# Kernel optimization log

Measured on AMD Instinct MI355X. Metric: run time of the kernel, lower is better.

## Reference

```python
import jax, jax.numpy as jnp
import numpy as np

B, S, D, H = 2, 2048, 1024, 16
DH = D // H
LEVELS, FACTOR = 3, 2


def setup_inputs() -> dict:
    key = jax.random.key(0)
    ks = jax.random.split(key, 12)
    s = 1.0 / np.sqrt(D)
    n = lambda k, shape, sc: (jax.random.normal(k, shape, jnp.float32) * sc)
    return {
        "query": n(ks[0], (B, S, D), 1.0),
        "key": n(ks[1], (B, S, D), 1.0),
        "value": n(ks[2], (B, S, D), 1.0),
        "Wq": n(ks[3], (D, D), s), "bq": jnp.zeros((D,), jnp.float32),
        "Wk": n(ks[4], (D, D), s), "bk": jnp.zeros((D,), jnp.float32),
        "Wv": n(ks[5], (D, D), s), "bv": jnp.zeros((D,), jnp.float32),
        "Wo": n(ks[6], (D, D), s), "bo": jnp.zeros((D,), jnp.float32),
        "w_levels": jnp.ones((LEVELS,), jnp.float32),
    }


def _downsample(m):
    # mean-pool pairs along sequence: [B, S, D] -> [B, S//FACTOR, D]
    b, s, d = m.shape
    sn = s // FACTOR
    return m[:, : sn * FACTOR, :].reshape(b, sn, FACTOR, d).mean(axis=2)


def _mha(q, k, v, Wq, bq, Wk, bk, Wv, bv, Wo, bo):
    b, sq, d = q.shape
    sk = k.shape[1]
    qh = (q @ Wq + bq).reshape(b, sq, H, DH)
    kh = (k @ Wk + bk).reshape(b, sk, H, DH)
    vh = (v @ Wv + bv).reshape(b, sk, H, DH)
    scores = jnp.einsum("bqhd,bkhd->bhqk", qh, kh) / np.sqrt(DH)
    attn = jax.nn.softmax(scores, axis=-1)
    out = jnp.einsum("bhqk,bkhd->bqhd", attn, vh).reshape(b, sq, d)
    return out @ Wo + bo


def reference(query, key, value, Wq, bq, Wk, bk, Wv, bv, Wo, bo, w_levels):
    keys, vals = [key], [value]
    k_, v_ = key, value
    for _ in range(LEVELS - 1):
        k_ = _downsample(k_)
        v_ = _downsample(v_)
        keys.append(k_)
        vals.append(v_)
    acc = None
    for lvl in range(LEVELS):
        o = _mha(query, keys[lvl], vals[lvl], Wq, bq, Wk, bk, Wv, bv, Wo, bo)
        o = o * w_levels[lvl]
        acc = o if acc is None else acc + o
    return acc / w_levels.sum()
```

## Files before the change

kernel.cpp:

```cpp
#include <hip/hip_runtime.h>


#define B_  2
#define S_  2048
#define D_  1024
#define H_  16
#define DH_ 64
#define THR2 10.0f

typedef short s8v __attribute__((ext_vector_type(8)));
typedef float f4v __attribute__((ext_vector_type(4)));
typedef float f16v __attribute__((ext_vector_type(16)));
typedef unsigned int u32x2 __attribute__((ext_vector_type(2)));
typedef unsigned int u32x4 __attribute__((ext_vector_type(4)));

__device__ __forceinline__ unsigned cvtpk(float lo, float hi){
    unsigned r;
    asm volatile("v_cvt_pk_bf16_f32 %0, %1, %2" : "=v"(r) : "v"(lo), "v"(hi));
    return r;
}
__device__ __forceinline__ unsigned short f2bf1(float v){
    unsigned r;
    asm volatile("v_cvt_pk_bf16_f32 %0, %1, %2" : "=v"(r) : "v"(v), "v"(v));
    return (unsigned short)r;
}
__device__ __forceinline__ float bf2f(unsigned short h){
    union { unsigned u; float f; } v; v.u = ((unsigned)h) << 16;
    return v.f;
}
__device__ __forceinline__ float exp2_(float x){
    float r; asm("v_exp_f32 %0, %1" : "=v"(r) : "v"(x)); return r;
}
__device__ __forceinline__ void pswap(unsigned &dst, unsigned &src){
    asm volatile("v_permlane32_swap_b32 %0, %1" : "+v"(dst), "+v"(src));
}
__device__ __forceinline__ unsigned addpk(unsigned x, unsigned y){
    union { unsigned u; float f; } a, b, c, d;
    a.u = x << 16;          b.u = y << 16;
    c.u = x & 0xFFFF0000u;  d.u = y & 0xFFFF0000u;
    return cvtpk(a.f + b.f, c.f + d.f);
}
__device__ __forceinline__ int swz(int row, int kb){
    return row*128 + (((kb) ^ (row & 7) ^ ((row >> 3) & 7)) << 4);
}

__global__ __launch_bounds__(256) void wtrans(
    const float* __restrict__ W0, const float* __restrict__ W1,
    const float* __restrict__ W2, const float* __restrict__ W3,
    unsigned short* __restrict__ T0, unsigned short* __restrict__ T1,
    unsigned short* __restrict__ T2, unsigned short* __restrict__ T3)
{
    __shared__ float tl[32][33];
    const float* W = blockIdx.z==0?W0: blockIdx.z==1?W1: blockIdx.z==2?W2:W3;
    unsigned short* T = blockIdx.z==0?T0: blockIdx.z==1?T1: blockIdx.z==2?T2:T3;
    const int t = threadIdx.x;
    const int bk = blockIdx.x*32, bn = blockIdx.y*32;
    {
        int row = t>>3, c4 = (t&7)*4;
        float4 v = *(const float4*)&W[(size_t)(bk+row)*D_ + bn + c4];
        tl[row][c4+0]=v.x; tl[row][c4+1]=v.y; tl[row][c4+2]=v.z; tl[row][c4+3]=v.w;
    }
    __syncthreads();
    {
        int n = t>>3, k4 = (t&7)*4;
        unsigned a = cvtpk(tl[k4+0][n], tl[k4+1][n]);
        unsigned b = cvtpk(tl[k4+2][n], tl[k4+3][n]);
        u32x2 pk = {a, b};
        *(u32x2*)&T[(size_t)(bn+n)*D_ + bk + k4] = pk;
    }
}

template<int MODE>
__global__ __launch_bounds__(256) void gemm_proj(
    const float* __restrict__ Af, const unsigned short* __restrict__ Btw,
    const float* __restrict__ bias, unsigned short* __restrict__ C, float scale)
{
    const int N_ = D_, K_ = D_;
    __shared__ __align__(16) char lds[65536];
    const int t = threadIdx.x;
    const int l = t & 63, wv = t>>6, g = l>>4, x = l&15;
    const int wr = wv>>1, wc = wv&1;
    const int br = blockIdx.y*128, bc = blockIdx.x*128;

    int rw[4], bl[4];
    #pragma unroll
    for (int p=0;p<4;++p){ int u = t + 256*p; rw[p] = u>>3; bl[p] = u&7; }

    f4v acc[4][4];
    #pragma unroll
    for (int i=0;i<4;++i)
        #pragma unroll
        for (int j=0;j<4;++j) acc[i][j] = (f4v){0.f,0.f,0.f,0.f};

    float4 alo[4], ahi[4]; s8v brg[4];
    #pragma unroll
    for (int p=0;p<4;++p){
        const float* ap = Af + (size_t)(br+rw[p])*K_ + bl[p]*8;
        alo[p] = *(const float4*)ap; ahi[p] = *(const float4*)(ap+4);
        brg[p] = *(const s8v*)(Btw + (size_t)(bc+rw[p])*K_ + bl[p]*8);
    }

    int cur = 0;
    for (int kt=0; kt<K_; kt+=64){
        char* AsB = lds + cur*32768;
        char* BsB = AsB + 16384;
        #pragma unroll
        for (int p=0;p<4;++p){
            uint4 pk;
            pk.x = cvtpk(alo[p].x, alo[p].y); pk.y = cvtpk(alo[p].z, alo[p].w);
            pk.z = cvtpk(ahi[p].x, ahi[p].y); pk.w = cvtpk(ahi[p].z, ahi[p].w);
            *(uint4*)(AsB + swz(rw[p], bl[p])) = pk;
            *(s8v*)(BsB + swz(rw[p], bl[p])) = brg[p];
        }
        if (kt + 64 < K_){
            #pragma unroll
            for (int p=0;p<4;++p){
                const float* ap = Af + (size_t)(br+rw[p])*K_ + (kt+64) + bl[p]*8;
                alo[p] = *(const float4*)ap; ahi[p] = *(const float4*)(ap+4);
                brg[p] = *(const s8v*)(Btw + (size_t)(bc+rw[p])*K_ + (kt+64) + bl[p]*8);
            }
        }
        __syncthreads();
        #pragma unroll
        for (int c=0;c<2;++c){
            s8v af[4], bf[4];
            #pragma unroll
            for (int fm=0; fm<4; ++fm)
                af[fm] = *(const s8v*)(AsB + swz(wr*64+fm*16+x, c*4+g));
            #pragma unroll
            for (int fn=0; fn<4; ++fn)
                bf[fn] = *(const s8v*)(BsB + swz(wc*64+fn*16+x, c*4+g));
            __builtin_amdgcn_s_setprio(1);
            #pragma unroll
            for (int fm=0; fm<4; ++fm)
                #pragma unroll
                for (int fn=0; fn<4; ++fn)
                    acc[fm][fn] = __builtin_amdgcn_mfma_f32_16x16x32_bf16(
                        af[fm], bf[fn], acc[fm][fn], 0,0,0);
            __builtin_amdgcn_s_setprio(0);
        }
        cur ^= 1;
    }

    #pragma unroll
    for (int fn=0; fn<4; ++fn){
        int col = bc + wc*64 + fn*16 + x;
        float bv = bias[col];
        #pragma unroll
        for (int fm=0; fm<4; ++fm){
            int row0 = br + wr*64 + fm*16 + g*4;
            float v0 = acc[fm][fn][0] + bv;
            float v1 = acc[fm][fn][1] + bv;
            float v2 = acc[fm][fn][2] + bv;
            float v3 = acc[fm][fn][3] + bv;
            if (MODE == 1){
                int hI = col>>6, dhI = col & (DH_-1);
                #pragma unroll
                for (int r=0;r<4;++r){
                    int row = row0 + r;
                    int bI = row>>11, sI = row & (S_-1);
                    float vv = (r==0?v0: r==1?v1: r==2?v2: v3) * scale;
                    C[(((size_t)(bI*H_+hI))*S_+sI)*DH_+dhI] = f2bf1(vv);
                }
            } else {
                int bI = row0>>11, sI = row0 & (S_-1);
                int hI = col>>6, dhI = col & (DH_-1);
                u32x2 pk;
                pk.x = cvtpk(v0*scale, v1*scale);
                pk.y = cvtpk(v2*scale, v3*scale);
                *(u32x2*)&C[(((size_t)(bI*H_+hI))*DH_+dhI)*S_ + sI] = pk;
            }
        }
    }
}

__global__ __launch_bounds__(256) void gemm_sum(
    const unsigned short* __restrict__ A0, const unsigned short* __restrict__ A1,
    const unsigned short* __restrict__ Btw, const float* __restrict__ bias,
    float* __restrict__ C)
{
    const int N_ = D_, K_ = D_;
    __shared__ __align__(16) char lds[65536];
    const int t = threadIdx.x;
    const int l = t & 63, wv = t>>6, g = l>>4, x = l&15;
    const int wr = wv>>1, wc = wv&1;
    const int br = blockIdx.y*128, bc = blockIdx.x*128;

    int rw[4], bl[4];
    #pragma unroll
    for (int p=0;p<4;++p){ int u = t + 256*p; rw[p] = u>>3; bl[p] = u&7; }

    f4v acc[4][4];
    #pragma unroll
    for (int i=0;i<4;++i)
        #pragma unroll
        for (int j=0;j<4;++j) acc[i][j] = (f4v){0.f,0.f,0.f,0.f};

    u32x4 a0r[4], a1r[4]; s8v brg[4];
    #pragma unroll
    for (int p=0;p<4;++p){
        a0r[p] = *(const u32x4*)(A0 + (size_t)(br+rw[p])*K_ + bl[p]*8);
        a1r[p] = *(const u32x4*)(A1 + (size_t)(br+rw[p])*K_ + bl[p]*8);
        brg[p] = *(const s8v*)(Btw + (size_t)(bc+rw[p])*K_ + bl[p]*8);
    }

    int cur = 0;
    for (int kt=0; kt<K_; kt+=64){
        char* AsB = lds + cur*32768;
        char* BsB = AsB + 16384;
        #pragma unroll
        for (int p=0;p<4;++p){
            uint4 pk;
            pk.x = addpk(a0r[p].x, a1r[p].x);
            pk.y = addpk(a0r[p].y, a1r[p].y);
            pk.z = addpk(a0r[p].z, a1r[p].z);
            pk.w = addpk(a0r[p].w, a1r[p].w);
            *(uint4*)(AsB + swz(rw[p], bl[p])) = pk;
            *(s8v*)(BsB + swz(rw[p], bl[p])) = brg[p];
        }
        if (kt + 64 < K_){
            #pragma unroll
            for (int p=0;p<4;++p){
                a0r[p] = *(const u32x4*)(A0 + (size_t)(br+rw[p])*K_ + (kt+64) + bl[p]*8);
                a1r[p] = *(const u32x4*)(A1 + (size_t)(br+rw[p])*K_ + (kt+64) + bl[p]*8);
                brg[p] = *(const s8v*)(Btw + (size_t)(bc+rw[p])*K_ + (kt+64) + bl[p]*8);
            }
        }
        __syncthreads();
        #pragma unroll
        for (int c=0;c<2;++c){
            s8v af[4], bf[4];
            #pragma unroll
            for (int fm=0; fm<4; ++fm)
                af[fm] = *(const s8v*)(AsB + swz(wr*64+fm*16+x, c*4+g));
            #pragma unroll
            for (int fn=0; fn<4; ++fn)
                bf[fn] = *(const s8v*)(BsB + swz(wc*64+fn*16+x, c*4+g));
            __builtin_amdgcn_s_setprio(1);
            #pragma unroll
            for (int fm=0; fm<4; ++fm)
                #pragma unroll
                for (int fn=0; fn<4; ++fn)
                    acc[fm][fn] = __builtin_amdgcn_mfma_f32_16x16x32_bf16(
                        af[fm], bf[fn], acc[fm][fn], 0,0,0);
            __builtin_amdgcn_s_setprio(0);
        }
        cur ^= 1;
    }

    #pragma unroll
    for (int fn=0; fn<4; ++fn){
        int col = bc + wc*64 + fn*16 + x;
        float bv = bias[col];
        #pragma unroll
        for (int fm=0; fm<4; ++fm){
            int row0 = br + wr*64 + fm*16 + g*4;
            #pragma unroll
            for (int r=0;r<4;++r)
                C[(size_t)(row0+r)*N_ + col] = acc[fm][fn][r] + bv;
        }
    }
}

__global__ __launch_bounds__(256) void pool_pair(
    const unsigned short* __restrict__ kin, unsigned short* __restrict__ kout,
    const unsigned short* __restrict__ vin, unsigned short* __restrict__ vout,
    int nOut4, int Sin, int shift)
{
    int idx = blockIdx.x * 256 + threadIdx.x;
    if (idx >= nOut4) return;
    if (blockIdx.z == 0){
        int d0 = (idx & 15) * 4;
        int rest = idx >> 4;
        int Sout = Sin >> 1;
        int so = rest % Sout, bh = rest / Sout;
        size_t base = ((size_t)bh * Sin + 2*so) * DH_ + d0;
        ushort4 a = *(const ushort4*)&kin[base];
        ushort4 c = *(const ushort4*)&kin[base + DH_];
        ushort4 o;
        o.x = f2bf1(0.5f*(bf2f(a.x)+bf2f(c.x)));
        o.y = f2bf1(0.5f*(bf2f(a.y)+bf2f(c.y)));
        o.z = f2bf1(0.5f*(bf2f(a.z)+bf2f(c.z)));
        o.w = f2bf1(0.5f*(bf2f(a.w)+bf2f(c.w)));
        *(ushort4*)&kout[(size_t)idx*4] = o;
    } else {
        int row = idx >> shift;
        int so4 = (idx & ((1<<shift)-1)) << 2;
        union { u32x4 u; unsigned short hh[8]; } a;
        a.u = *(const u32x4*)&vin[(size_t)row*Sin + so4*2];
        float m0 = 0.5f*(bf2f(a.hh[0])+bf2f(a.hh[1]));
        float m1 = 0.5f*(bf2f(a.hh[2])+bf2f(a.hh[3]));
        float m2 = 0.5f*(bf2f(a.hh[4])+bf2f(a.hh[5]));
        float m3 = 0.5f*(bf2f(a.hh[6])+bf2f(a.hh[7]));
        u32x2 pk; pk.x = cvtpk(m0,m1); pk.y = cvtpk(m2,m3);
        *(u32x2*)&vout[(size_t)row*(Sin>>1) + so4] = pk;
    }
}

__global__ __launch_bounds__(256, 2) void attn_mfma7(
    const unsigned short* __restrict__ qh,
    const unsigned short* __restrict__ kh0, const unsigned short* __restrict__ kh1,
    const unsigned short* __restrict__ kh2,
    const unsigned short* __restrict__ vt0, const unsigned short* __restrict__ vt1,
    const unsigned short* __restrict__ vt2,
    const float* __restrict__ wlv,
    unsigned short* __restrict__ acc0, unsigned short* __restrict__ acc1)
{
    __shared__ __align__(16) char ksm[2][8192];
    __shared__ __align__(16) char vsm[2][8192];
    const int t = threadIdx.x, l = t&63, wv = t>>6, q = l&31, hi = l>>5;
    const int bid = blockIdx.x;
    const int qt = bid & 15, h = (bid>>4) & (H_-1), b = bid >> 8;
    const int grp = blockIdx.y;
    const int lvB = grp ? 1 : 0, lvE = grp ? 3 : 1;
    unsigned short* accOut = grp ? acc1 : acc0;

    const float w0 = wlv[0], w1 = wlv[1], w2 = wlv[2];
    const float winv = 1.f/(w0+w1+w2);

    const unsigned short* qp =
        qh + (((size_t)(b*H_+h))*S_ + (size_t)qt*128 + wv*32 + q)*DH_ + hi*8;
    s8v qf0 = *(const s8v*)(qp);
    s8v qf1 = *(const s8v*)(qp + 16);
    s8v qf2 = *(const s8v*)(qp + 32);
    s8v qf3 = *(const s8v*)(qp + 48);

    const int r0 = t>>3, kb = t&7;
    const int off0 = swz(r0, kb), off1 = swz(r0+32, kb);

    f16v aO0, aO1;
    #pragma unroll
    for (int r=0;r<16;++r){ aO0[r]=0.f; aO1[r]=0.f; }

    int cur = 0;
    #pragma unroll 1
    for (int lvl = lvB; lvl < lvE; ++lvl) {
        const unsigned short *kp, *vpt; int nt; float wc;
        if (lvl == 0)      { kp = kh0; vpt = vt0; nt = 32; wc = w0; }
        else if (lvl == 1) { kp = kh1; vpt = vt1; nt = 16; wc = w1; }
        else               { kp = kh2; vpt = vt2; nt = 8;  wc = w2; }
        const int Sl = nt*64;
        const unsigned short* kbase = kp + (size_t)(b*H_+h)*Sl*DH_;
        const unsigned short* v0r = vpt + ((size_t)(b*H_+h)*DH_ + r0)*Sl;
        const unsigned short* v1r = vpt + ((size_t)(b*H_+h)*DH_ + r0+32)*Sl;

        float m_i = -1e30f, l_i = 0.f;
        f16v o0, o1;
        #pragma unroll
        for (int r=0;r<16;++r){ o0[r]=0.f; o1[r]=0.f; }

        s8v krg0 = *(const s8v*)(kbase + (size_t)r0*DH_ + kb*8);
        s8v krg1 = *(const s8v*)(kbase + (size_t)(r0+32)*DH_ + kb*8);
        s8v vrg0 = *(const s8v*)(v0r + kb*8);
        s8v vrg1 = *(const s8v*)(v1r + kb*8);

        for (int kt = 0; kt < nt; ++kt) {
            char* kb_ = ksm[cur];
            char* vb_ = vsm[cur];
            *(s8v*)(kb_ + off0) = krg0;
            *(s8v*)(kb_ + off1) = krg1;
            *(s8v*)(vb_ + off0) = vrg0;
            *(s8v*)(vb_ + off1) = vrg1;
            if (kt + 1 < nt) {
                size_t nb = (size_t)(kt+1)*64;
                krg0 = *(const s8v*)(kbase + (nb+r0)*DH_ + kb*8);
                krg1 = *(const s8v*)(kbase + (nb+r0+32)*DH_ + kb*8);
                vrg0 = *(const s8v*)(v0r + nb + kb*8);
                vrg1 = *(const s8v*)(v1r + nb + kb*8);
            }
            __syncthreads();

            f16v s0, s1;
            #pragma unroll
            for (int r=0;r<16;++r){ s0[r]=0.f; s1[r]=0.f; }
            {
                s8v k00 = *(const s8v*)(kb_ + swz(q,      0*2+hi));
                s8v k01 = *(const s8v*)(kb_ + swz(q,      1*2+hi));
                s8v k02 = *(const s8v*)(kb_ + swz(q,      2*2+hi));
                s8v k03 = *(const s8v*)(kb_ + swz(q,      3*2+hi));
                s8v k10 = *(const s8v*)(kb_ + swz(32+q,   0*2+hi));
                s8v k11 = *(const s8v*)(kb_ + swz(32+q,   1*2+hi));
                s8v k12 = *(const s8v*)(kb_ + swz(32+q,   2*2+hi));
                s8v k13 = *(const s8v*)(kb_ + swz(32+q,   3*2+hi));
                __builtin_amdgcn_s_setprio(1);
                s0 = __builtin_amdgcn_mfma_f32_32x32x16_bf16(k00, qf0, s0, 0,0,0);
                s1 = __builtin_amdgcn_mfma_f32_32x32x16_bf16(k10, qf0, s1, 0,0,0);
                s0 = __builtin_amdgcn_mfma_f32_32x32x16_bf16(k01, qf1, s0, 0,0,0);
                s1 = __builtin_amdgcn_mfma_f32_32x32x16_bf16(k11, qf1, s1, 0,0,0);
                s0 = __builtin_amdgcn_mfma_f32_32x32x16_bf16(k02, qf2, s0, 0,0,0);
                s1 = __builtin_amdgcn_mfma_f32_32x32x16_bf16(k12, qf2, s1, 0,0,0);
                s0 = __builtin_amdgcn_mfma_f32_32x32x16_bf16(k03, qf3, s0, 0,0,0);
                s1 = __builtin_amdgcn_mfma_f32_32x32x16_bf16(k13, qf3, s1, 0,0,0);
                __builtin_amdgcn_s_setprio(0);
            }

            float pm = s0[0];
            #pragma unroll
            for (int r=1;r<16;++r) pm = fmaxf(pm, s0[r]);
            #pragma unroll
            for (int r=0;r<16;++r) pm = fmaxf(pm, s1[r]);
            pm = fmaxf(pm, __shfl_xor(pm, 32, 64));
            if (__any(pm > m_i + THR2)) {
                float mn = fmaxf(m_i, pm);
                float corr = exp2_(m_i - mn);
                m_i = mn;
                l_i *= corr;
                #pragma unroll
                for (int r=0;r<16;++r){
                    float cb = __shfl(corr, ((r&3)+8*(r>>2)) + 4*hi, 64);
                    o0[r] *= cb; o1[r] *= cb;
                }
            }
            float rs = 0.f;
            #pragma unroll
            for (int r=0;r<16;++r){ s0[r] = exp2_(s0[r]-m_i); rs += s0[r]; }
            #pragma unroll
            for (int r=0;r<16;++r){ s1[r] = exp2_(s1[r]-m_i); rs += s1[r]; }
            rs += __shfl_xor(rs, 32, 64);
            l_i += rs;

            unsigned a0 = cvtpk(s0[0], s0[1]),  a1 = cvtpk(s0[2], s0[3]);
            unsigned b0 = cvtpk(s0[4], s0[5]),  b1 = cvtpk(s0[6], s0[7]);
            pswap(a0, b0); pswap(a1, b1);
            unsigned c0 = cvtpk(s0[8], s0[9]),  c1 = cvtpk(s0[10], s0[11]);
            unsigned d0 = cvtpk(s0[12], s0[13]),d1 = cvtpk(s0[14], s0[15]);
            pswap(c0, d0); pswap(c1, d1);
            unsigned e0 = cvtpk(s1[0], s1[1]),  e1 = cvtpk(s1[2], s1[3]);
            unsigned f0 = cvtpk(s1[4], s1[5]),  f1 = cvtpk(s1[6], s1[7]);
            pswap(e0, f0); pswap(e1, f1);
            unsigned g0 = cvtpk(s1[8], s1[9]),  g1 = cvtpk(s1[10], s1[11]);
            unsigned h0 = cvtpk(s1[12], s1[13]),h1 = cvtpk(s1[14], s1[15]);
            pswap(g0, h0); pswap(g1, h1);
            union { u32x4 u; s8v s; } pf0, pf1, pf2, pf3;
            pf0.u = (u32x4){a0, a1, b0, b1};
            pf1.u = (u32x4){c0, c1, d0, d1};
            pf2.u = (u32x4){e0, e1, f0, f1};
            pf3.u = (u32x4){g0, g1, h0, h1};

            {
                s8v v00 = *(const s8v*)(vb_ + swz(q,    0*2+hi));
                s8v v01 = *(const s8v*)(vb_ + swz(q,    1*2+hi));
                s8v v02 = *(const s8v*)(vb_ + swz(q,    2*2+hi));
                s8v v03 = *(const s8v*)(vb_ + swz(q,    3*2+hi));
                s8v v10 = *(const s8v*)(vb_ + swz(32+q, 0*2+hi));
                s8v v11 = *(const s8v*)(vb_ + swz(32+q, 1*2+hi));
                s8v v12 = *(const s8v*)(vb_ + swz(32+q, 2*2+hi));
                s8v v13 = *(const s8v*)(vb_ + swz(32+q, 3*2+hi));
                __builtin_amdgcn_s_setprio(1);
                o0 = __builtin_amdgcn_mfma_f32_32x32x16_bf16(pf0.s, v00, o0, 0,0,0);
                o1 = __builtin_amdgcn_mfma_f32_32x32x16_bf16(pf0.s, v10, o1, 0,0,0);
                o0 = __builtin_amdgcn_mfma_f32_32x32x16_bf16(pf1.s, v01, o0, 0,0,0);
                o1 = __builtin_amdgcn_mfma_f32_32x32x16_bf16(pf1.s, v11, o1, 0,0,0);
                o0 = __builtin_amdgcn_mfma_f32_32x32x16_bf16(pf2.s, v02, o0, 0,0,0);
                o1 = __builtin_amdgcn_mfma_f32_32x32x16_bf16(pf2.s, v12, o1, 0,0,0);
                o0 = __builtin_amdgcn_mfma_f32_32x32x16_bf16(pf3.s, v03, o0, 0,0,0);
                o1 = __builtin_amdgcn_mfma_f32_32x32x16_bf16(pf3.s, v13, o1, 0,0,0);
                __builtin_amdgcn_s_setprio(0);
            }
            cur ^= 1;
        }

        float wl = wc * winv;
        #pragma unroll
        for (int r=0;r<16;++r){
            float lb = __shfl(l_i, ((r&3)+8*(r>>2)) + 4*hi, 64);
            float sc = wl / lb;
            aO0[r] += o0[r] * sc;
            aO1[r] += o1[r] * sc;
        }
    }

    #pragma unroll
    for (int r=0;r<16;++r){
        int qrow = ((r&3)+8*(r>>2)) + 4*hi;
        size_t row = (size_t)b*S_ + (size_t)qt*128 + wv*32 + qrow;
        accOut[row*D_ + h*DH_ + q]      = f2bf1(aO0[r]);
        accOut[row*D_ + h*DH_ + 32 + q] = f2bf1(aO1[r]);
    }
}

extern "C" void kernel_launch(void* const* d_in, const int* in_sizes, int n_in,
                              void* d_out, int out_size, void* d_ws, size_t ws_size,
                              hipStream_t stream)
{
    const float* query = (const float*)d_in[0];
    const float* key   = (const float*)d_in[1];
    const float* value = (const float*)d_in[2];
    const float* Wq = (const float*)d_in[3];  const float* bq = (const float*)d_in[4];
    const float* Wk = (const float*)d_in[5];  const float* bk = (const float*)d_in[6];
    const float* Wv = (const float*)d_in[7];  const float* bv = (const float*)d_in[8];
    const float* Wo = (const float*)d_in[9];  const float* bo = (const float*)d_in[10];
    const float* wlv = (const float*)d_in[11];

    char* w = (char*)d_ws;
    unsigned short* qhb  = (unsigned short*)(w);
    unsigned short* khb0 = (unsigned short*)(w + 8388608);
    unsigned short* khb1 = (unsigned short*)(w + 16777216);
    unsigned short* khb2 = (unsigned short*)(w + 20971520);
    unsigned short* vtb0 = (unsigned short*)(w + 23068672);
    unsigned short* vtb1 = (unsigned short*)(w + 31457280);
    unsigned short* vtb2 = (unsigned short*)(w + 35651584);
    unsigned short* acc0 = (unsigned short*)(w + 37748736);
    unsigned short* Wto  = (unsigned short*)(w + 46137344);
    unsigned short* Wtq  = (unsigned short*)(w + 48234496);
    unsigned short* Wtk  = (unsigned short*)(w + 50331648);
    unsigned short* Wtv  = (unsigned short*)(w + 52428800);
    unsigned short* acc1 = (unsigned short*)(w + 48234496);

    dim3 bb(256);
    wtrans<<<dim3(32,32,4), bb, 0, stream>>>(Wq, Wk, Wv, Wo, Wtq, Wtk, Wtv, Wto);

    const float scale_q = 0.125f * 1.44269504088896f;
    dim3 gg(D_/128, (B_*S_)/128);
    gemm_proj<1><<<gg, bb, 0, stream>>>(query, Wtq, bq, qhb,  scale_q);
    gemm_proj<1><<<gg, bb, 0, stream>>>(key,   Wtk, bk, khb0, 1.0f);
    gemm_proj<2><<<gg, bb, 0, stream>>>(value, Wtv, bv, vtb0, 1.0f);

    int n1 = B_ * H_ * (S_/2) * DH_ / 4;
    int n2 = B_ * H_ * (S_/4) * DH_ / 4;
    pool_pair<<<dim3(n1/256,1,2), bb, 0, stream>>>(khb0, khb1, vtb0, vtb1, n1, S_,   8);
    pool_pair<<<dim3(n2/256,1,2), bb, 0, stream>>>(khb1, khb2, vtb1, vtb2, n2, S_/2, 7);

    attn_mfma7<<<dim3(512, 2), bb, 0, stream>>>(qhb, khb0, khb1, khb2,
                                                vtb0, vtb1, vtb2, wlv, acc0, acc1);

    gemm_sum<<<gg, bb, 0, stream>>>(acc0, acc1, Wto, bo, (float*)d_out);
}
```

Measured before the change: 194.0 us.

## Split attention per level, batch QKV projections, sum three accumulators in output GEMM

After: 196.2 us. No clear change (+1.1%).

```diff
diff --git a/kernel.cpp b/kernel.cpp
--- a/kernel.cpp
+++ b/kernel.cpp
@@ -31,14 +31,18 @@
 __device__ __forceinline__ float exp2_(float x){
     float r; asm("v_exp_f32 %0, %1" : "=v"(r) : "v"(x)); return r;
 }
+__device__ __forceinline__ float max3_(float a, float b, float c){
+    float r; asm("v_max3_f32 %0, %1, %2, %3" : "=v"(r) : "v"(a), "v"(b), "v"(c));
+    return r;
+}
 __device__ __forceinline__ void pswap(unsigned &dst, unsigned &src){
     asm volatile("v_permlane32_swap_b32 %0, %1" : "+v"(dst), "+v"(src));
 }
-__device__ __forceinline__ unsigned addpk(unsigned x, unsigned y){
-    union { unsigned u; float f; } a, b, c, d;
-    a.u = x << 16;          b.u = y << 16;
-    c.u = x & 0xFFFF0000u;  d.u = y & 0xFFFF0000u;
-    return cvtpk(a.f + b.f, c.f + d.f);
+__device__ __forceinline__ unsigned addpk3(unsigned x, unsigned y, unsigned z){
+    union { unsigned u; float f; } xl, yl, zl, xh, yh, zh;
+    xl.u = x << 16;          yl.u = y << 16;          zl.u = z << 16;
+    xh.u = x & 0xFFFF0000u;  yh.u = y & 0xFFFF0000u;  zh.u = z & 0xFFFF0000u;
+    return cvtpk(xl.f + yl.f + zl.f, xh.f + yh.f + zh.f);
 }
 __device__ __forceinline__ int swz(int row, int kb){
     return row*128 + (((kb) ^ (row & 7) ^ ((row >> 3) & 7)) << 4);
@@ -70,16 +74,26 @@
     }
 }
 
-template<int MODE>
-__global__ __launch_bounds__(256) void gemm_proj(
-    const float* __restrict__ Af, const unsigned short* __restrict__ Btw,
-    const float* __restrict__ bias, unsigned short* __restrict__ C, float scale)
+__global__ __launch_bounds__(256) void gemm_qkv3(
+    const float* __restrict__ Aq, const float* __restrict__ Ak, const float* __restrict__ Avv,
+    const unsigned short* __restrict__ Wq_, const unsigned short* __restrict__ Wk_,
+    const unsigned short* __restrict__ Wv_,
+    const float* __restrict__ bq_, const float* __restrict__ bk_, const float* __restrict__ bv_,
+    unsigned short* __restrict__ Oq, unsigned short* __restrict__ Ok,
+    unsigned short* __restrict__ Ov, float scale_q)
 {
+    const int z = blockIdx.z;
+    const float* Af = z==0?Aq : z==1?Ak : Avv;
+    const unsigned short* Btw = z==0?Wq_ : z==1?Wk_ : Wv_;
+    const float* bias = z==0?bq_ : z==1?bk_ : bv_;
+    unsigned short* C = z==0?Oq : z==1?Ok : Ov;
+    const float scale = z==0? scale_q : 1.0f;
+
     const int N_ = D_, K_ = D_;
     __shared__ __align__(16) char lds[65536];
     const int t = threadIdx.x;
-    const int l = t & 63, wv = t>>6, g = l>>4, x = l&15;
-    const int wr = wv>>1, wc = wv&1;
+    const int l = t & 63, wvi = t>>6, g = l>>4, x = l&15;
+    const int wr = wvi>>1, wc = wvi&1;
     const int br = blockIdx.y*128, bc = blockIdx.x*128;
 
     int rw[4], bl[4];
@@ -153,7 +167,7 @@
             float v1 = acc[fm][fn][1] + bv;
             float v2 = acc[fm][fn][2] + bv;
             float v3 = acc[fm][fn][3] + bv;
-            if (MODE == 1){
+            if (z != 2){
                 int hI = col>>6, dhI = col & (DH_-1);
                 #pragma unroll
                 for (int r=0;r<4;++r){
@@ -166,8 +180,8 @@
                 int bI = row0>>11, sI = row0 & (S_-1);
                 int hI = col>>6, dhI = col & (DH_-1);
                 u32x2 pk;
-                pk.x = cvtpk(v0*scale, v1*scale);
-                pk.y = cvtpk(v2*scale, v3*scale);
+                pk.x = cvtpk(v0, v1);
+                pk.y = cvtpk(v2, v3);
                 *(u32x2*)&C[(((size_t)(bI*H_+hI))*DH_+dhI)*S_ + sI] = pk;
             }
         }
@@ -176,14 +190,14 @@
 
 __global__ __launch_bounds__(256) void gemm_sum(
     const unsigned short* __restrict__ A0, const unsigned short* __restrict__ A1,
-    const unsigned short* __restrict__ Btw, const float* __restrict__ bias,
-    float* __restrict__ C)
+    const unsigned short* __restrict__ A2, const unsigned short* __restrict__ Btw,
+    const float* __restrict__ bias, float* __restrict__ C)
 {
     const int N_ = D_, K_ = D_;
     __shared__ __align__(16) char lds[65536];
     const int t = threadIdx.x;
-    const int l = t & 63, wv = t>>6, g = l>>4, x = l&15;
-    const int wr = wv>>1, wc = wv&1;
+    const int l = t & 63, wvi = t>>6, g = l>>4, x = l&15;
+    const int wr = wvi>>1, wc = wvi&1;
     const int br = blockIdx.y*128, bc = blockIdx.x*128;
 
     int rw[4], bl[4];
@@ -196,11 +210,13 @@
         #pragma unroll
         for (int j=0;j<4;++j) acc[i][j] = (f4v){0.f,0.f,0.f,0.f};
 
-    u32x4 a0r[4], a1r[4]; s8v brg[4];
+    u32x4 a0r[4], a1r[4], a2r[4]; s8v brg[4];
     #pragma unroll
     for (int p=0;p<4;++p){
-        a0r[p] = *(const u32x4*)(A0 + (size_t)(br+rw[p])*K_ + bl[p]*8);
-        a1r[p] = *(const u32x4*)(A1 + (size_t)(br+rw[p])*K_ + bl[p]*8);
+        size_t off = (size_t)(br+rw[p])*K_ + bl[p]*8;
+        a0r[p] = *(const u32x4*)(A0 + off);
+        a1r[p] = *(const u32x4*)(A1 + off);
+        a2r[p] = *(const u32x4*)(A2 + off);
         brg[p] = *(const s8v*)(Btw + (size_t)(bc+rw[p])*K_ + bl[p]*8);
     }
 
@@ -211,18 +227,20 @@
         #pragma unroll
         for (int p=0;p<4;++p){
             uint4 pk;
-            pk.x = addpk(a0r[p].x, a1r[p].x);
-            pk.y = addpk(a0r[p].y, a1r[p].y);
-            pk.z = addpk(a0r[p].z, a1r[p].z);
-            pk.w = addpk(a0r[p].w, a1r[p].w);
+            pk.x = addpk3(a0r[p].x, a1r[p].x, a2r[p].x);
+            pk.y = addpk3(a0r[p].y, a1r[p].y, a2r[p].y);
+            pk.z = addpk3(a0r[p].z, a1r[p].z, a2r[p].z);
+            pk.w = addpk3(a0r[p].w, a1r[p].w, a2r[p].w);
             *(uint4*)(AsB + swz(rw[p], bl[p])) = pk;
             *(s8v*)(BsB + swz(rw[p], bl[p])) = brg[p];
         }
         if (kt + 64 < K_){
             #pragma unroll
             for (int p=0;p<4;++p){
-                a0r[p] = *(const u32x4*)(A0 + (size_t)(br+rw[p])*K_ + (kt+64) + bl[p]*8);
-                a1r[p] = *(const u32x4*)(A1 + (size_t)(br+rw[p])*K_ + (kt+64) + bl[p]*8);
+                size_t off = (size_t)(br+rw[p])*K_ + (kt+64) + bl[p]*8;
+                a0r[p] = *(const u32x4*)(A0 + off);
+                a1r[p] = *(const u32x4*)(A1 + off);
+                a2r[p] = *(const u32x4*)(A2 + off);
                 brg[p] = *(const s8v*)(Btw + (size_t)(bc+rw[p])*K_ + (kt+64) + bl[p]*8);
             }
         }
@@ -297,26 +315,29 @@
     }
 }
 
-__global__ __launch_bounds__(256, 2) void attn_mfma7(
+__global__ __launch_bounds__(256, 3) void attn_mfma8(
     const unsigned short* __restrict__ qh,
     const unsigned short* __restrict__ kh0, const unsigned short* __restrict__ kh1,
     const unsigned short* __restrict__ kh2,
     const unsigned short* __restrict__ vt0, const unsigned short* __restrict__ vt1,
     const unsigned short* __restrict__ vt2,
     const float* __restrict__ wlv,
-    unsigned short* __restrict__ acc0, unsigned short* __restrict__ acc1)
+    unsigned short* __restrict__ acc0, unsigned short* __restrict__ acc1,
+    unsigned short* __restrict__ acc2)
 {
     __shared__ __align__(16) char ksm[2][8192];
     __shared__ __align__(16) char vsm[2][8192];
     const int t = threadIdx.x, l = t&63, wv = t>>6, q = l&31, hi = l>>5;
     const int bid = blockIdx.x;
     const int qt = bid & 15, h = (bid>>4) & (H_-1), b = bid >> 8;
-    const int grp = blockIdx.y;
-    const int lvB = grp ? 1 : 0, lvE = grp ? 3 : 1;
-    unsigned short* accOut = grp ? acc1 : acc0;
+    const int lvl = blockIdx.y;
+    const int nt = 32 >> lvl;
+    const unsigned short* kp  = lvl==0 ? kh0 : (lvl==1 ? kh1 : kh2);
+    const unsigned short* vpt = lvl==0 ? vt0 : (lvl==1 ? vt1 : vt2);
+    unsigned short* accOut    = lvl==0 ? acc0 : (lvl==1 ? acc1 : acc2);
 
     const float w0 = wlv[0], w1 = wlv[1], w2 = wlv[2];
-    const float winv = 1.f/(w0+w1+w2);
+    const float wl = wlv[lvl] / (w0 + w1 + w2);
 
     const unsigned short* qp =
         qh + (((size_t)(b*H_+h))*S_ + (size_t)qt*128 + wv*32 + q)*DH_ + hi*8;
@@ -328,154 +349,148 @@
     const int r0 = t>>3, kb = t&7;
     const int off0 = swz(r0, kb), off1 = swz(r0+32, kb);
 
-    f16v aO0, aO1;
-    #pragma unroll
-    for (int r=0;r<16;++r){ aO0[r]=0.f; aO1[r]=0.f; }
+    const int Sl = nt*64;
+    const unsigned short* kbase = kp + (size_t)(b*H_+h)*Sl*DH_;
+    const unsigned short* v0r = vpt + ((size_t)(b*H_+h)*DH_ + r0)*Sl;
+    const unsigned short* v1r = vpt + ((size_t)(b*H_+h)*DH_ + r0+32)*Sl;
+
+    float m_i = -1e30f, l_i = 0.f;
+    f16v o0, o1;
+    #pragma unroll
+    for (int r=0;r<16;++r){ o0[r]=0.f; o1[r]=0.f; }
+
+    s8v krg0 = *(const s8v*)(kbase + (size_t)r0*DH_ + kb*8);
+    s8v krg1 = *(const s8v*)(kbase + (size_t)(r0+32)*DH_ + kb*8);
+    s8v vrg0 = *(const s8v*)(v0r + kb*8);
+    s8v vrg1 = *(const s8v*)(v1r + kb*8);
 
     int cur = 0;
-    #pragma unroll 1
-    for (int lvl = lvB; lvl < lvE; ++lvl) {
-        const unsigned short *kp, *vpt; int nt; float wc;
-        if (lvl == 0)      { kp = kh0; vpt = vt0; nt = 32; wc = w0; }
-        else if (lvl == 1) { kp = kh1; vpt = vt1; nt = 16; wc = w1; }
-        else               { kp = kh2; vpt = vt2; nt = 8;  wc = w2; }
-        const int Sl = nt*64;
-        const unsigned short* kbase = kp + (size_t)(b*H_+h)*Sl*DH_;
-        const unsigned short* v0r = vpt + ((size_t)(b*H_+h)*DH_ + r0)*Sl;
-        const unsigned short* v1r = vpt + ((size_t)(b*H_+h)*DH_ + r0+32)*Sl;
-
-        float m_i = -1e30f, l_i = 0.f;
-        f16v o0, o1;
-        #pragma unroll
-        for (int r=0;r<16;++r){ o0[r]=0.f; o1[r]=0.f; }
-
-        s8v krg0 = *(const s8v*)(kbase + (size_t)r0*DH_ + kb*8);
-        s8v krg1 = *(const s8v*)(kbase + (size_t)(r0+32)*DH_ + kb*8);
-        s8v vrg0 = *(const s8v*)(v0r + kb*8);
-        s8v vrg1 = *(const s8v*)(v1r + kb*8);
-
-        for (int kt = 0; kt < nt; ++kt) {
-            char* kb_ = ksm[cur];
-            char* vb_ = vsm[cur];
-            *(s8v*)(kb_ + off0) = krg0;
-            *(s8v*)(kb_ + off1) = krg1;
-            *(s8v*)(vb_ + off0) = vrg0;
-            *(s8v*)(vb_ + off1) = vrg1;
-            if (kt + 1 < nt) {
-                size_t nb = (size_t)(kt+1)*64;
-                krg0 = *(const s8v*)(kbase + (nb+r0)*DH_ + kb*8);
-                krg1 = *(const s8v*)(kbase + (nb+r0+32)*DH_ + kb*8);
-                vrg0 = *(const s8v*)(v0r + nb + kb*8);
-                vrg1 = *(const s8v*)(v1r + nb + kb*8);
+    for (int kt = 0; kt < nt; ++kt) {
+        char* kb_ = ksm[cur];
+        char* vb_ = vsm[cur];
+        *(s8v*)(kb_ + off0) = krg0;
+        *(s8v*)(kb_ + off1) = krg1;
+        *(s8v*)(vb_ + off0) = vrg0;
+        *(s8v*)(vb_ + off1) = vrg1;
+        if (kt + 1 < nt) {
+            size_t nb = (size_t)(kt+1)*64;
+            krg0 = *(const s8v*)(kbase + (nb+r0)*DH_ + kb*8);
+            krg1 = *(const s8v*)(kbase + (nb+r0+32)*DH_ + kb*8);
+            vrg0 = *(const s8v*)(v0r + nb + kb*8);
+            vrg1 = *(const s8v*)(v1r + nb + kb*8);
+        }
+        __syncthreads();
+
+        f16v s0, s1;
+        #pragma unroll
+        for (int r=0;r<16;++r){ s0[r]=0.f; s1[r]=0.f; }
+        {
+            s8v k00 = *(const s8v*)(kb_ + swz(q,      0*2+hi));
+            s8v k01 = *(const s8v*)(kb_ + swz(q,      1*2+hi));
+            s8v k02 = *(const s8v*)(kb_ + swz(q,      2*2+hi));
+            s8v k03 = *(const s8v*)(kb_ + swz(q,      3*2+hi));
+            s8v k10 = *(const s8v*)(kb_ + swz(32+q,   0*2+hi));
+            s8v k11 = *(const s8v*)(kb_ + swz(32+q,   1*2+hi));
+            s8v k12 = *(const s8v*)(kb_ + swz(32+q,   2*2+hi));
+            s8v k13 = *(const s8v*)(kb_ + swz(32+q,   3*2+hi));
+            __builtin_amdgcn_s_setprio(1);
+            s0 = __builtin_amdgcn_mfma_f32_32x32x16_bf16(k00, qf0, s0, 0,0,0);
+            s1 = __builtin_amdgcn_mfma_f32_32x32x16_bf16(k10, qf0, s1, 0,0,0);
+            s0 = __builtin_amdgcn_mfma_f32_32x32x16_bf16(k01, qf1, s0, 0,0,0);
+            s1 = __builtin_amdgcn_mfma_f32_32x32x16_bf16(k11, qf1, s1, 0,0,0);
+            s0 = __builtin_amdgcn_mfma_f32_32x32x16_bf16(k02, qf2, s0, 0,0,0);
+            s1 = __builtin_amdgcn_mfma_f32_32x32x16_bf16(k12, qf2, s1, 0,0,0);
+            s0 = __builtin_amdgcn_mfma_f32_32x32x16_bf16(k03, qf3, s0, 0,0,0);
+            s1 = __builtin_amdgcn_mfma_f32_32x32x16_bf16(k13, qf3, s1, 0,0,0);
+            __builtin_amdgcn_s_setprio(0);
+        }
+
+        float ca = max3_(s0[0], s0[1], s0[2]);
+        ca = max3_(ca, s0[3], s0[4]);
+        ca = max3_(ca, s0[5], s0[6]);
+        ca = fmaxf(ca, s0[7]);
+        float cb = max3_(s0[8], s0[9], s0[10]);
+        cb = max3_(cb, s0[11], s0[12]);
+        cb = max3_(cb, s0[13], s0[14]);
+        cb = fmaxf(cb, s0[15]);
+        float cc = max3_(s1[0], s1[1], s1[2]);
+        cc = max3_(cc, s1[3], s1[4]);
+        cc = max3_(cc, s1[5], s1[6]);
+        cc = fmaxf(cc, s1[7]);
+        float cd = max3_(s1[8], s1[9], s1[10]);
+        cd = max3_(cd, s1[11], s1[12]);
+        cd = max3_(cd, s1[13], s1[14]);
+        cd = fmaxf(cd, s1[15]);
+        float pm = fmaxf(max3_(ca, cb, cc), cd);
+        pm = fmaxf(pm, __shfl_xor(pm, 32, 64));
+        if (__any(pm > m_i + THR2)) {
+            float mn = fmaxf(m_i, pm);
+            float corr = exp2_(m_i - mn);
+            m_i = mn;
+            l_i *= corr;
+            #pragma unroll
+            for (int r=0;r<16;++r){
+                float cbc = __shfl(corr, ((r&3)+8*(r>>2)) + 4*hi, 64);
+                o0[r] *= cbc; o1[r] *= cbc;
             }
-            __syncthreads();
-
-            f16v s0, s1;
-            #pragma unroll
-            for (int r=0;r<16;++r){ s0[r]=0.f; s1[r]=0.f; }
-            {
-                s8v k00 = *(const s8v*)(kb_ + swz(q,      0*2+hi));
-                s8v k01 = *(const s8v*)(kb_ + swz(q,      1*2+hi));
-                s8v k02 = *(const s8v*)(kb_ + swz(q,      2*2+hi));
-                s8v k03 = *(const s8v*)(kb_ + swz(q,      3*2+hi));
-                s8v k10 = *(const s8v*)(kb_ + swz(32+q,   0*2+hi));
-                s8v k11 = *(const s8v*)(kb_ + swz(32+q,   1*2+hi));
-                s8v k12 = *(const s8v*)(kb_ + swz(32+q,   2*2+hi));
-                s8v k13 = *(const s8v*)(kb_ + swz(32+q,   3*2+hi));
-                __builtin_amdgcn_s_setprio(1);
-                s0 = __builtin_amdgcn_mfma_f32_32x32x16_bf16(k00, qf0, s0, 0,0,0);
-                s1 = __builtin_amdgcn_mfma_f32_32x32x16_bf16(k10, qf0, s1, 0,0,0);
-                s0 = __builtin_amdgcn_mfma_f32_32x32x16_bf16(k01, qf1, s0, 0,0,0);
-                s1 = __builtin_amdgcn_mfma_f32_32x32x16_bf16(k11, qf1, s1, 0,0,0);
-                s0 = __builtin_amdgcn_mfma_f32_32x32x16_bf16(k02, qf2, s0, 0,0,0);
-                s1 = __builtin_amdgcn_mfma_f32_32x32x16_bf16(k12, qf2, s1, 0,0,0);
-                s0 = __builtin_amdgcn_mfma_f32_32x32x16_bf16(k03, qf3, s0, 0,0,0);
-                s1 = __builtin_amdgcn_mfma_f32_32x32x16_bf16(k13, qf3, s1, 0,0,0);
-                __builtin_amdgcn_s_setprio(0);
-            }
-
-            float pm = s0[0];
-            #pragma unroll
-            for (int r=1;r<16;++r) pm = fmaxf(pm, s0[r]);
-            #pragma unroll
-            for (int r=0;r<16;++r) pm = fmaxf(pm, s1[r]);
-            pm = fmaxf(pm, __shfl_xor(pm, 32, 64));
-            if (__any(pm > m_i + THR2)) {
-                float mn = fmaxf(m_i, pm);
-                float corr = exp2_(m_i - mn);
-                m_i = mn;
-                l_i *= corr;
-                #pragma unroll
-                for (int r=0;r<16;++r){
-                    float cb = __shfl(corr, ((r&3)+8*(r>>2)) + 4*hi, 64);
-                    o0[r] *= cb; o1[r] *= cb;
-                }
-            }
-            float rs = 0.f;
-            #pragma unroll
-            for (int r=0;r<16;++r){ s0[r] = exp2_(s0[r]-m_i); rs += s0[r]; }
-            #pragma unroll
-            for (int r=0;r<16;++r){ s1[r] = exp2_(s1[r]-m_i); rs += s1[r]; }
-            rs += __shfl_xor(rs, 32, 64);
-            l_i += rs;
-
-            unsigned a0 = cvtpk(s0[0], s0[1]),  a1 = cvtpk(s0[2], s0[3]);
-            unsigned b0 = cvtpk(s0[4], s0[5]),  b1 = cvtpk(s0[6], s0[7]);
-            pswap(a0, b0); pswap(a1, b1);
-            unsigned c0 = cvtpk(s0[8], s0[9]),  c1 = cvtpk(s0[10], s0[11]);
-            unsigned d0 = cvtpk(s0[12], s0[13]),d1 = cvtpk(s0[14], s0[15]);
-            pswap(c0, d0); pswap(c1, d1);
-            unsigned e0 = cvtpk(s1[0], s1[1]),  e1 = cvtpk(s1[2], s1[3]);
-            unsigned f0 = cvtpk(s1[4], s1[5]),  f1 = cvtpk(s1[6], s1[7]);
-            pswap(e0, f0); pswap(e1, f1);
-            unsigned g0 = cvtpk(s1[8], s1[9]),  g1 = cvtpk(s1[10], s1[11]);
-            unsigned h0 = cvtpk(s1[12], s1[13]),h1 = cvtpk(s1[14], s1[15]);
-            pswap(g0, h0); pswap(g1, h1);
-            union { u32x4 u; s8v s; } pf0, pf1, pf2, pf3;
-            pf0.u = (u32x4){a0, a1, b0, b1};
-            pf1.u = (u32x4){c0, c1, d0, d1};
-            pf2.u = (u32x4){e0, e1, f0, f1};
-            pf3.u = (u32x4){g0, g1, h0, h1};
-
-            {
-                s8v v00 = *(const s8v*)(vb_ + swz(q,    0*2+hi));
-                s8v v01 = *(const s8v*)(vb_ + swz(q,    1*2+hi));
-                s8v v02 = *(const s8v*)(vb_ + swz(q,    2*2+hi));
-                s8v v03 = *(const s8v*)(vb_ + swz(q,    3*2+hi));
-                s8v v10 = *(const s8v*)(vb_ + swz(32+q, 0*2+hi));
-                s8v v11 = *(const s8v*)(vb_ + swz(32+q, 1*2+hi));
-                s8v v12 = *(const s8v*)(vb_ + swz(32+q, 2*2+hi));
-                s8v v13 = *(const s8v*)(vb_ + swz(32+q, 3*2+hi));
-                __builtin_amdgcn_s_setprio(1);
-                o0 = __builtin_amdgcn_mfma_f32_32x32x16_bf16(pf0.s, v00, o0, 0,0,0);
-                o1 = __builtin_amdgcn_mfma_f32_32x32x16_bf16(pf0.s, v10, o1, 0,0,0);
-                o0 = __builtin_amdgcn_mfma_f32_32x32x16_bf16(pf1.s, v01, o0, 0,0,0);
-                o1 = __builtin_amdgcn_mfma_f32_32x32x16_bf16(pf1.s, v11, o1, 0,0,0);
-                o0 = __builtin_amdgcn_mfma_f32_32x32x16_bf16(pf2.s, v02, o0, 0,0,0);
-                o1 = __builtin_amdgcn_mfma_f32_32x32x16_bf16(pf2.s, v12, o1, 0,0,0);
-                o0 = __builtin_amdgcn_mfma_f32_32x32x16_bf16(pf3.s, v03, o0, 0,0,0);
-                o1 = __builtin_amdgcn_mfma_f32_32x32x16_bf16(pf3.s, v13, o1, 0,0,0);
-                __builtin_amdgcn_s_setprio(0);
-            }
-            cur ^= 1;
-        }
-
-        float wl = wc * winv;
-        #pragma unroll
-        for (int r=0;r<16;++r){
-            float lb = __shfl(l_i, ((r&3)+8*(r>>2)) + 4*hi, 64);
-            float sc = wl / lb;
-            aO0[r] += o0[r] * sc;
-            aO1[r] += o1[r] * sc;
-        }
+        }
+        float rs = 0.f;
+        #pragma unroll
+        for (int r=0;r<16;++r){ s0[r] = exp2_(s0[r]-m_i); rs += s0[r]; }
+        #pragma unroll
+        for (int r=0;r<16;++r){ s1[r] = exp2_(s1[r]-m_i); rs += s1[r]; }
+        rs += __shfl_xor(rs, 32, 64);
+        l_i += rs;
+
+        unsigned a0 = cvtpk(s0[0], s0[1]),  a1 = cvtpk(s0[2], s0[3]);
+        unsigned b0 = cvtpk(s0[4], s0[5]),  b1 = cvtpk(s0[6], s0[7]);
+        pswap(a0, b0); pswap(a1, b1);
+        unsigned c0 = cvtpk(s0[8], s0[9]),  c1 = cvtpk(s0[10], s0[11]);
+        unsigned d0 = cvtpk(s0[12], s0[13]),d1 = cvtpk(s0[14], s0[15]);
+        pswap(c0, d0); pswap(c1, d1);
+        unsigned e0 = cvtpk(s1[0], s1[1]),  e1 = cvtpk(s1[2], s1[3]);
+        unsigned f0 = cvtpk(s1[4], s1[5]),  f1 = cvtpk(s1[6], s1[7]);
+        pswap(e0, f0); pswap(e1, f1);
+        unsigned g0 = cvtpk(s1[8], s1[9]),  g1 = cvtpk(s1[10], s1[11]);
+        unsigned h0 = cvtpk(s1[12], s1[13]),h1 = cvtpk(s1[14], s1[15]);
+        pswap(g0, h0); pswap(g1, h1);
+        union { u32x4 u; s8v s; } pf0, pf1, pf2, pf3;
+        pf0.u = (u32x4){a0, a1, b0, b1};
+        pf1.u = (u32x4){c0, c1, d0, d1};
+        pf2.u = (u32x4){e0, e1, f0, f1};
+        pf3.u = (u32x4){g0, g1, h0, h1};
+
+        {
+            s8v v00 = *(const s8v*)(vb_ + swz(q,    0*2+hi));
+            s8v v01 = *(const s8v*)(vb_ + swz(q,    1*2+hi));
+            s8v v02 = *(const s8v*)(vb_ + swz(q,    2*2+hi));
+            s8v v03 = *(const s8v*)(vb_ + swz(q,    3*2+hi));
+            s8v v10 = *(const s8v*)(vb_ + swz(32+q, 0*2+hi));
+            s8v v11 = *(const s8v*)(vb_ + swz(32+q, 1*2+hi));
+            s8v v12 = *(const s8v*)(vb_ + swz(32+q, 2*2+hi));
+            s8v v13 = *(const s8v*)(vb_ + swz(32+q, 3*2+hi));
+            __builtin_amdgcn_s_setprio(1);
+            o0 = __builtin_amdgcn_mfma_f32_32x32x16_bf16(pf0.s, v00, o0, 0,0,0);
+            o1 = __builtin_amdgcn_mfma_f32_32x32x16_bf16(pf0.s, v10, o1, 0,0,0);
+            o0 = __builtin_amdgcn_mfma_f32_32x32x16_bf16(pf1.s, v01, o0, 0,0,0);
+            o1 = __builtin_amdgcn_mfma_f32_32x32x16_bf16(pf1.s, v11, o1, 0,0,0);
+            o0 = __builtin_amdgcn_mfma_f32_32x32x16_bf16(pf2.s, v02, o0, 0,0,0);
+            o1 = __builtin_amdgcn_mfma_f32_32x32x16_bf16(pf2.s, v12, o1, 0,0,0);
+            o0 = __builtin_amdgcn_mfma_f32_32x32x16_bf16(pf3.s, v03, o0, 0,0,0);
+            o1 = __builtin_amdgcn_mfma_f32_32x32x16_bf16(pf3.s, v13, o1, 0,0,0);
+            __builtin_amdgcn_s_setprio(0);
+        }
+        cur ^= 1;
     }
 
     #pragma unroll
     for (int r=0;r<16;++r){
         int qrow = ((r&3)+8*(r>>2)) + 4*hi;
+        float lb = __shfl(l_i, qrow, 64);
+        float sc = wl / lb;
         size_t row = (size_t)b*S_ + (size_t)qt*128 + wv*32 + qrow;
-        accOut[row*D_ + h*DH_ + q]      = f2bf1(aO0[r]);
-        accOut[row*D_ + h*DH_ + 32 + q] = f2bf1(aO1[r]);
+        accOut[row*D_ + h*DH_ + q]      = f2bf1(o0[r] * sc);
+        accOut[row*D_ + h*DH_ + 32 + q] = f2bf1(o1[r] * sc);
     }
 }
 
@@ -500,29 +515,30 @@
     unsigned short* vtb0 = (unsigned short*)(w + 23068672);
     unsigned short* vtb1 = (unsigned short*)(w + 31457280);
     unsigned short* vtb2 = (unsigned short*)(w + 35651584);
-    unsigned short* acc0 = (unsigned short*)(w + 37748736);
-    unsigned short* Wto  = (unsigned short*)(w + 46137344);
-    unsigned short* Wtq  = (unsigned short*)(w + 48234496);
-    unsigned short* Wtk  = (unsigned short*)(w + 50331648);
-    unsigned short* Wtv  = (unsigned short*)(w + 52428800);
+    unsigned short* Wto  = (unsigned short*)(w + 37748736);
+    unsigned short* Wtq  = (unsigned short*)(w + 39845888);
+    unsigned short* Wtk  = (unsigned short*)(w + 41943040);
+    unsigned short* Wtv  = (unsigned short*)(w + 44040192);
+    unsigned short* acc0 = (unsigned short*)(w + 39845888);
     unsigned short* acc1 = (unsigned short*)(w + 48234496);
+    unsigned short* acc2 = (unsigned short*)(w + 56623104);
 
     dim3 bb(256);
     wtrans<<<dim3(32,32,4), bb, 0, stream>>>(Wq, Wk, Wv, Wo, Wtq, Wtk, Wtv, Wto);
 
     const float scale_q = 0.125f * 1.44269504088896f;
-    dim3 gg(D_/128, (B_*S_)/128);
-    gemm_proj<1><<<gg, bb, 0, stream>>>(query, Wtq, bq, qhb,  scale_q);
-    gemm_proj<1><<<gg, bb, 0, stream>>>(key,   Wtk, bk, khb0, 1.0f);
-    gemm_proj<2><<<gg, bb, 0, stream>>>(value, Wtv, bv, vtb0, 1.0f);
+    gemm_qkv3<<<dim3(8, 32, 3), bb, 0, stream>>>(query, key, value,
+                                                 Wtq, Wtk, Wtv, bq, bk, bv,
+                                                 qhb, khb0, vtb0, scale_q);
 
     int n1 = B_ * H_ * (S_/2) * DH_ / 4;
     int n2 = B_ * H_ * (S_/4) * DH_ / 4;
     pool_pair<<<dim3(n1/256,1,2), bb, 0, stream>>>(khb0, khb1, vtb0, vtb1, n1, S_,   8);
     pool_pair<<<dim3(n2/256,1,2), bb, 0, stream>>>(khb1, khb2, vtb1, vtb2, n2, S_/2, 7);
 
-    attn_mfma7<<<dim3(512, 2), bb, 0, stream>>>(qhb, khb0, khb1, khb2,
-                                                vtb0, vtb1, vtb2, wlv, acc0, acc1);
-
-    gemm_sum<<<gg, bb, 0, stream>>>(acc0, acc1, Wto, bo, (float*)d_out);
-}
+    attn_mfma8<<<dim3(512, 3), bb, 0, stream>>>(qhb, khb0, khb1, khb2,
+                                                vtb0, vtb1, vtb2, wlv,
+                                                acc0, acc1, acc2);
+
+    gemm_sum<<<dim3(8, 32), bb, 0, stream>>>(acc0, acc1, acc2, Wto, bo, (float*)d_out);
+}
```
